# Kernel tuning notes

Measured on AMD Instinct MI355X. Metric: run time of the kernel, lower is better.

Reference implementation:

```python
import jax, jax.numpy as jnp
import numpy as np

N = 100000      # nodes
E = 1600000     # edges (avg degree 16)
D = 128         # in_feats
C = 40          # n_classes
K = 4           # propagation steps
T = 2.0
DELTA = T / K   # 0.5
EPS = 1e-5      # LayerNorm eps


def setup_inputs() -> dict:
    key = jax.random.key(0)
    k1, k2, k3, k4, k5 = jax.random.split(key, 5)
    feat = jax.random.normal(k1, (N, D), jnp.float32)
    row = jax.random.randint(k2, (E,), 0, N, dtype=jnp.int32)
    col = jax.random.randint(k3, (E,), 0, N, dtype=jnp.int32)
    # fc: Linear(D -> C), xavier-ish scale
    W = jax.random.normal(k4, (C, D), jnp.float32) / np.sqrt(D)
    b = jax.random.normal(k5, (C,), jnp.float32) * 0.01
    # LayerNorm params
    gamma = jnp.ones((C,), jnp.float32)
    beta = jnp.zeros((C,), jnp.float32)
    return {"feat": feat, "row": row, "col": col, "W": W, "b": b,
            "gamma": gamma, "beta": beta}


def reference(feat, row, col, W, b, gamma, beta):
    # degrees of augmented adjacency A + I (row counts + self loop)
    deg = jnp.zeros((N,), feat.dtype).at[row].add(1.0) + 1.0
    dinv = jax.lax.rsqrt(deg)
    w_edge = dinv[row] * dinv[col]     # S[row,col] for off-diagonal entries
    w_self = dinv * dinv               # S[i,i] from the added self loop
    # h <- ((1-delta) I + delta S)^K @ feat, applied iteratively (same math as
    # precomputing the matrix power, but never materializes it)
    h = feat
    for _ in range(K):
        agg = jax.ops.segment_sum(h[col] * w_edge[:, None], row, num_segments=N)
        agg = agg + h * w_self[:, None]
        h = (1.0 - DELTA) * h + DELTA * agg
    # fc
    h = h @ W.T + b                    # [N, C]
    # LayerNorm over last dim
    mu = jnp.mean(h, axis=-1, keepdims=True)
    var = jnp.var(h, axis=-1, keepdims=True)
    h = (h - mu) * jax.lax.rsqrt(var + EPS) * gamma + beta
    return h
```

## Files before the change

kernel.cpp:

```cpp
#include <hip/hip_runtime.h>
#include <hip/hip_fp16.h>

#define N_NODES 100000
#define N_EDGES 1600000
#define D_FEAT  128
#define C_CLS   40
#define ZSTRIDE 32
#define LN_EPS  1e-5f

#define RPB   256
#define NBKT  ((N_NODES + RPB - 1) / RPB)
#define BCAP  6144
#define TILE_E 4096
#define EBLK  ((N_EDGES + TILE_E - 1) / TILE_E)
#define NTILES (N_NODES / 16)
#define FCB   ((NTILES + 3) / 4)

typedef __attribute__((ext_vector_type(8))) _Float16 half8;
typedef __attribute__((ext_vector_type(4))) float floatx4;
typedef __attribute__((ext_vector_type(2))) float floatx2;
typedef __attribute__((ext_vector_type(2))) int   intx2;
typedef __attribute__((ext_vector_type(4))) unsigned uintx4;

__device__ inline float2 h2f2(unsigned v) {
    __half2 h = *(__half2*)&v;
    return __half22float2(h);
}
__device__ inline unsigned f2h2(float x, float y) {
    __half2 h = __floats2half2_rn(x, y);
    return *(unsigned*)&h;
}

__global__ __launch_bounds__(256) void init_k(const float* __restrict__ W,
                                              _Float16* __restrict__ wh,
                                              int* __restrict__ bktsz,
                                              unsigned* __restrict__ z0,
                                              unsigned* __restrict__ z1) {
    int t = threadIdx.x;
    if (blockIdx.x < 20) {
        int i = blockIdx.x * 256 + t;
        if (i < C_CLS * D_FEAT) wh[i] = (_Float16)W[i];
        return;
    }
    for (int i = t; i < NBKT; i += 256) bktsz[i] = 0;
    if (t < ZSTRIDE) {
        z0[(size_t)N_NODES * ZSTRIDE + t] = 0u;
        z1[(size_t)N_NODES * ZSTRIDE + t] = 0u;
    }
}

__global__ __launch_bounds__(256) void fcbin_k(const float* __restrict__ feat,
                                               const _Float16* __restrict__ wh,
                                               const int* __restrict__ row,
                                               const int* __restrict__ col,
                                               int* __restrict__ bktsz,
                                               int* __restrict__ csr_tmp,
                                               unsigned* __restrict__ z) {
    __shared__ int hist[NBKT];
    __shared__ int cbase[NBKT];
    __shared__ _Float16 zl[4][16][72];
    int t = threadIdx.x;
    if (blockIdx.x < EBLK) {
        int tile = blockIdx.x * TILE_E;
        for (int i = t; i < NBKT; i += 256) hist[i] = 0;
        __syncthreads();
        int r[16], c[16], pos[16];
        #pragma unroll
        for (int k = 0; k < 16; k++) {
            int e = tile + k * 256 + t;
            if (e < N_EDGES) {
                r[k] = row[e]; c[k] = col[e];
                pos[k] = atomicAdd(&hist[r[k] / RPB], 1);
            } else r[k] = -1;
        }
        __syncthreads();
        for (int i = t; i < NBKT; i += 256) {
            int h = hist[i];
            cbase[i] = h ? atomicAdd(&bktsz[i], h) : 0;
        }
        __syncthreads();
        #pragma unroll
        for (int k = 0; k < 16; k++) {
            if (r[k] >= 0) {
                int b = r[k] / RPB;
                int slot = cbase[b] + pos[k];
                if (slot < BCAP)
                    csr_tmp[b * BCAP + slot] = ((r[k] & (RPB - 1)) << 17) | c[k];
            }
        }
        return;
    }
    int wave = t >> 6, lane = t & 63;
    int m = lane & 15, quad = lane >> 4;
    int tile = (blockIdx.x - EBLK) * 4 + wave;
    bool valid = (tile < NTILES);
    int node0 = tile * 16;

    half8 bfrag[3][4];
    if (valid) {
        const half8* wh8 = (const half8*)wh;
        #pragma unroll
        for (int ct = 0; ct < 3; ct++) {
            int c = ct * 16 + m;
            bool ok = (c < C_CLS);
            #pragma unroll
            for (int ks = 0; ks < 4; ks++) {
                if (ok) {
                    bfrag[ct][ks] = wh8[c * 16 + ks * 4 + quad];
                } else {
                    #pragma unroll
                    for (int j = 0; j < 8; j++) bfrag[ct][ks][j] = (_Float16)0.0f;
                }
            }
        }
    }

    floatx4 acc0 = {0.f,0.f,0.f,0.f}, acc1 = acc0, acc2 = acc0;
    if (valid) {
        #pragma unroll
        for (int ks = 0; ks < 4; ks++) {
            const float4* ap = (const float4*)&feat[(node0 + m) * D_FEAT + ks * 32 + quad * 8];
            float4 a0 = ap[0], a1 = ap[1];
            half8 afrag;
            afrag[0] = (_Float16)a0.x; afrag[1] = (_Float16)a0.y;
            afrag[2] = (_Float16)a0.z; afrag[3] = (_Float16)a0.w;
            afrag[4] = (_Float16)a1.x; afrag[5] = (_Float16)a1.y;
            afrag[6] = (_Float16)a1.z; afrag[7] = (_Float16)a1.w;
            acc0 = __builtin_amdgcn_mfma_f32_16x16x32_f16(afrag, bfrag[0][ks], acc0, 0, 0, 0);
            acc1 = __builtin_amdgcn_mfma_f32_16x16x32_f16(afrag, bfrag[1][ks], acc1, 0, 0, 0);
            acc2 = __builtin_amdgcn_mfma_f32_16x16x32_f16(afrag, bfrag[2][ks], acc2, 0, 0, 0);
        }
    }

    {
        int zr = lane >> 2;
        uint2 zz = make_uint2(0u, 0u);
        ((uint2*)&zl[wave][zr][48])[lane & 3] = zz;
    }
    if (valid) {
        #pragma unroll
        for (int r = 0; r < 4; r++) {
            int zrow = quad * 4 + r;
            zl[wave][zrow][m]      = (_Float16)acc0[r];
            zl[wave][zrow][16 + m] = (_Float16)acc1[r];
            zl[wave][zrow][32 + m] = (_Float16)acc2[r];
        }
    }
    __syncthreads();
    if (valid) {
        int zr = lane >> 2, part = lane & 3;
        uint4 v0 = ((uint4*)&zl[wave][zr][0])[part];
        uint4 v1 = ((uint4*)&zl[wave][zr][0])[part + 4];
        uint4* zg = (uint4*)z;
        zg[(size_t)(node0 + zr) * 8 + part]     = v0;
        zg[(size_t)(node0 + zr) * 8 + part + 4] = v1;
    }
}

__global__ __launch_bounds__(256) void refine_k(const int* __restrict__ csr_tmp,
                                                const int* __restrict__ bktsz,
                                                int2* __restrict__ rowinfo,
                                                float2* __restrict__ rowc,
                                                int* __restrict__ csr_col,
                                                unsigned* __restrict__ z) {
    __shared__ int hist[RPB];
    __shared__ int psc[RPB];
    __shared__ int cur[RPB];
    __shared__ float dl[RPB];
    int b = blockIdx.x, t = threadIdx.x;
    int r0 = b * RPB;
    int nrows = min(RPB, N_NODES - r0);
    hist[t] = 0;
    __syncthreads();
    int cnt = bktsz[b];
    const int* base = csr_tmp + b * BCAP;
    for (int i = t; i < cnt; i += 256)
        atomicAdd(&hist[base[i] >> 17], 1);
    __syncthreads();
    int v = hist[t];
    psc[t] = v;
    __syncthreads();
    for (int off = 1; off < 256; off <<= 1) {
        int x = (t >= off) ? psc[t - off] : 0;
        __syncthreads();
        psc[t] += x;
        __syncthreads();
    }
    int start = b * BCAP + psc[t] - v;
    cur[t] = start;
    float fdeg = (float)v + 1.0f;
    float inv  = 1.0f / fdeg;
    dl[t] = rsqrtf(fdeg);
    if (t < nrows) {
        rowinfo[r0 + t] = make_int2(start, start + v);
        rowc[r0 + t]    = make_float2(0.5f + 0.5f * inv,
                                      0.5f * inv);
    }
    __syncthreads();
    for (int i = t; i < cnt; i += 256) {
        int pk = base[i];
        int lr = pk >> 17;
        int p = atomicAdd(&cur[lr], 1);
        csr_col[p] = pk & 0x1FFFF;
    }
    int total = nrows * ZSTRIDE;
    unsigned* zb = z + (size_t)r0 * ZSTRIDE;
    for (int i = t; i < total; i += 256) {
        float s = dl[i >> 5];
        float2 f = h2f2(zb[i]);
        zb[i] = f2h2(f.x * s, f.y * s);
    }
}

template<bool FINAL>
__global__ __launch_bounds__(256) void prop_u_t(const unsigned* __restrict__ hin,
                                                unsigned* __restrict__ hout,
                                                const int2* __restrict__ rowinfo,
                                                const float2* __restrict__ rowc,
                                                const int* __restrict__ csr_col,
                                                const float* __restrict__ bias,
                                                const float* __restrict__ gamma,
                                                const float* __restrict__ beta,
                                                float* __restrict__ out) {
    int t = threadIdx.x;
    int wave = t >> 6, lane = t & 63;
    int q   = lane >> 3;
    int sub = lane & 7;
    int node = blockIdx.x * 32 + wave * 8 + q;
    const uintx4* hin4 = (const uintx4*)hin;

    uintx4 hv = hin4[(unsigned)node * 8 + sub];
    floatx2 rc = __builtin_nontemporal_load((const floatx2*)rowc + node);
    float acc[8] = {0.f,0.f,0.f,0.f,0.f,0.f,0.f,0.f};

    intx2 ri = __builtin_nontemporal_load((const intx2*)rowinfo + node);
    int j = ri.x, end = ri.y;
    int base = ri.x;

    int e[8];
    #pragma unroll
    for (int k = 0; k < 8; k++)
        e[k] = __builtin_nontemporal_load(csr_col + ((j + k < end) ? j + k : base));

    while (__any(j < end)) {
        uintx4 g[8];
        #pragma unroll
        for (int k = 0; k < 8; k++) {
            int c = (j + k < end) ? e[k] : N_NODES;
            g[k] = hin4[(unsigned)c * 8 + sub];
        }
        int j2 = j + 8;
        #pragma unroll
        for (int k = 0; k < 8; k++)
            e[k] = __builtin_nontemporal_load(csr_col + ((j2 + k < end) ? j2 + k : base));
        #pragma unroll
        for (int k = 0; k < 8; k++) {
            float2 f0 = h2f2(g[k].x), f1 = h2f2(g[k].y), f2 = h2f2(g[k].z), f3 = h2f2(g[k].w);
            acc[0] += f0.x; acc[1] += f0.y;
            acc[2] += f1.x; acc[3] += f1.y;
            acc[4] += f2.x; acc[5] += f2.y;
            acc[6] += f3.x; acc[7] += f3.y;
        }
        j = j2;
    }

    float2 h0 = h2f2(hv.x), h1 = h2f2(hv.y), h2 = h2f2(hv.z), h3 = h2f2(hv.w);
    float r8[8];
    r8[0] = rc.x * h0.x + rc.y * acc[0]; r8[1] = rc.x * h0.y + rc.y * acc[1];
    r8[2] = rc.x * h1.x + rc.y * acc[2]; r8[3] = rc.x * h1.y + rc.y * acc[3];
    r8[4] = rc.x * h2.x + rc.y * acc[4]; r8[5] = rc.x * h2.y + rc.y * acc[5];
    r8[6] = rc.x * h3.x + rc.y * acc[6]; r8[7] = rc.x * h3.y + rc.y * acc[7];

    if (!FINAL) {
        uintx4 o;
        o.x = f2h2(r8[0], r8[1]);
        o.y = f2h2(r8[2], r8[3]);
        o.z = f2h2(r8[4], r8[5]);
        o.w = f2h2(r8[6], r8[7]);
        ((uintx4*)hout)[(unsigned)node * 8 + sub] = o;
    } else {
        float fs = rsqrtf(2.0f * rc.x - 1.0f);
        bool realsub = (sub < 5);
        int cb = sub * 8;
        float vv[8];
        float s = 0.0f, ss = 0.0f;
        #pragma unroll
        for (int i = 0; i < 8; i++) {
            float x = realsub ? (fs * r8[i] + bias[cb + i]) : 0.0f;
            vv[i] = x;
            s += x; ss += x * x;
        }
        s  += __shfl_xor(s, 1);  s  += __shfl_xor(s, 2);  s  += __shfl_xor(s, 4);
        ss += __shfl_xor(ss, 1); ss += __shfl_xor(ss, 2); ss += __shfl_xor(ss, 4);
        float mean = s * (1.0f / C_CLS);
        float var  = ss * (1.0f / C_CLS) - mean * mean;
        float inv  = rsqrtf(var + LN_EPS);
        if (realsub) {
            float o8[8];
            #pragma unroll
            for (int i = 0; i < 8; i++)
                o8[i] = (vv[i] - mean) * inv * gamma[cb + i] + beta[cb + i];
            float* orow = out + (size_t)node * C_CLS + cb;
            ((float4*)orow)[0] = make_float4(o8[0], o8[1], o8[2], o8[3]);
            ((float4*)orow)[1] = make_float4(o8[4], o8[5], o8[6], o8[7]);
        }
    }
}

extern "C" void kernel_launch(void* const* d_in, const int* in_sizes, int n_in,
                              void* d_out, int out_size, void* d_ws, size_t ws_size,
                              hipStream_t stream) {
    const float* feat  = (const float*)d_in[0];
    const int*   row   = (const int*)d_in[1];
    const int*   col   = (const int*)d_in[2];
    const float* W     = (const float*)d_in[3];
    const float* b     = (const float*)d_in[4];
    const float* gamma = (const float*)d_in[5];
    const float* beta  = (const float*)d_in[6];
    float* out = (float*)d_out;

    char* ws = (char*)d_ws;
    size_t off = 0;
    auto alloc = [&](size_t bytes) {
        size_t o = off;
        off = (off + bytes + 255) & ~(size_t)255;
        return o;
    };
    float2*   rowc     = (float2*)  (ws + alloc((size_t)N_NODES * 8));
    int2*     rowinfo  = (int2*)    (ws + alloc((size_t)N_NODES * 8));
    int*      bktsz    = (int*)     (ws + alloc((size_t)NBKT * 4));
    _Float16* wh       = (_Float16*)(ws + alloc((size_t)C_CLS * D_FEAT * 2));
    int*      csr_tmp  = (int*)     (ws + alloc((size_t)NBKT * BCAP * 4));
    int*      csr_col  = (int*)     (ws + alloc((size_t)NBKT * BCAP * 4));
    unsigned* z0       = (unsigned*)(ws + alloc((size_t)(N_NODES + 8) * ZSTRIDE * 4));
    unsigned* z1       = (unsigned*)(ws + alloc((size_t)(N_NODES + 8) * ZSTRIDE * 4));

    init_k<<<21, 256, 0, stream>>>(W, wh, bktsz, z0, z1);
    fcbin_k<<<EBLK + FCB, 256, 0, stream>>>(feat, wh, row, col, bktsz, csr_tmp, z0);
    refine_k<<<NBKT, 256, 0, stream>>>(csr_tmp, bktsz, rowinfo, rowc, csr_col, z0);

    int pgrid = N_NODES / 32;
    prop_u_t<false><<<pgrid, 256, 0, stream>>>(z0, z1, rowinfo, rowc, csr_col,
                                               nullptr, nullptr, nullptr, nullptr);
    prop_u_t<false><<<pgrid, 256, 0, stream>>>(z1, z0, rowinfo, rowc, csr_col,
                                               nullptr, nullptr, nullptr, nullptr);
    prop_u_t<false><<<pgrid, 256, 0, stream>>>(z0, z1, rowinfo, rowc, csr_col,
                                               nullptr, nullptr, nullptr, nullptr);
    prop_u_t<true><<<pgrid, 256, 0, stream>>>(z1, nullptr, rowinfo, rowc, csr_col,
                                              b, gamma, beta, out);
}
```

Baseline: 293.3 us.

## Split padded fp16 node features into compact lo/hi planes to cut gather bytes

The fp16 node-feature buffer changes from 128 bytes per node (40 used features padded to 64) to two planes: 32 features in a 64-byte row, and the remaining 8 features in a separate 16-byte-per-node region. The FC writer, the degree-scaling pass, the init code and the propagation gathers are all updated to address the two planes. This shrinks both the random-gather traffic and the working set of each propagation step. The nontemporal loads on the CSR and row metadata become ordinary loads. Lanes for sub-blocks 5–7 now redundantly load the hi plane, and the hi plane needs an extra 16-byte access per neighbour.

```diff
diff --git a/kernel.cpp b/kernel.cpp
--- a/kernel.cpp
+++ b/kernel.cpp
@@ -5,7 +5,6 @@
 #define N_EDGES 1600000
 #define D_FEAT  128
 #define C_CLS   40
-#define ZSTRIDE 32
 #define LN_EPS  1e-5f
 
 #define RPB   256
@@ -16,10 +15,12 @@
 #define NTILES (N_NODES / 16)
 #define FCB   ((NTILES + 3) / 4)
 
+#define ZPAD  8
+#define QLO   ((N_NODES + ZPAD) * 4)
+#define ZBYTES ((size_t)(N_NODES + ZPAD) * 80)
+
 typedef __attribute__((ext_vector_type(8))) _Float16 half8;
 typedef __attribute__((ext_vector_type(4))) float floatx4;
-typedef __attribute__((ext_vector_type(2))) float floatx2;
-typedef __attribute__((ext_vector_type(2))) int   intx2;
 typedef __attribute__((ext_vector_type(4))) unsigned uintx4;
 
 __device__ inline float2 h2f2(unsigned v) {
@@ -43,9 +44,13 @@
         return;
     }
     for (int i = t; i < NBKT; i += 256) bktsz[i] = 0;
-    if (t < ZSTRIDE) {
-        z0[(size_t)N_NODES * ZSTRIDE + t] = 0u;
-        z1[(size_t)N_NODES * ZSTRIDE + t] = 0u;
+    if (t < 16) {
+        z0[(size_t)N_NODES * 16 + t] = 0u;
+        z1[(size_t)N_NODES * 16 + t] = 0u;
+    }
+    if (t < 4) {
+        z0[(size_t)QLO * 4 + (size_t)N_NODES * 4 + t] = 0u;
+        z1[(size_t)QLO * 4 + (size_t)N_NODES * 4 + t] = 0u;
     }
 }
 
@@ -132,11 +137,6 @@
         }
     }
 
-    {
-        int zr = lane >> 2;
-        uint2 zz = make_uint2(0u, 0u);
-        ((uint2*)&zl[wave][zr][48])[lane & 3] = zz;
-    }
     if (valid) {
         #pragma unroll
         for (int r = 0; r < 4; r++) {
@@ -149,11 +149,12 @@
     __syncthreads();
     if (valid) {
         int zr = lane >> 2, part = lane & 3;
-        uint4 v0 = ((uint4*)&zl[wave][zr][0])[part];
-        uint4 v1 = ((uint4*)&zl[wave][zr][0])[part + 4];
-        uint4* zg = (uint4*)z;
-        zg[(size_t)(node0 + zr) * 8 + part]     = v0;
-        zg[(size_t)(node0 + zr) * 8 + part + 4] = v1;
+        uint4 lo = ((uint4*)&zl[wave][zr][0])[part];
+        ((uint4*)z)[(size_t)(node0 + zr) * 4 + part] = lo;
+        if (part == 0) {
+            uint4 hi = *(uint4*)&zl[wave][zr][32];
+            ((uint4*)z)[QLO + node0 + zr] = hi;
+        }
     }
 }
 
@@ -203,12 +204,19 @@
         int p = atomicAdd(&cur[lr], 1);
         csr_col[p] = pk & 0x1FFFF;
     }
-    int total = nrows * ZSTRIDE;
-    unsigned* zb = z + (size_t)r0 * ZSTRIDE;
-    for (int i = t; i < total; i += 256) {
-        float s = dl[i >> 5];
-        float2 f = h2f2(zb[i]);
-        zb[i] = f2h2(f.x * s, f.y * s);
+    int totlo = nrows * 16;
+    unsigned* zlo = z + (size_t)r0 * 16;
+    for (int i = t; i < totlo; i += 256) {
+        float s = dl[i >> 4];
+        float2 f = h2f2(zlo[i]);
+        zlo[i] = f2h2(f.x * s, f.y * s);
+    }
+    int tothi = nrows * 4;
+    unsigned* zhi = z + (size_t)QLO * 4 + (size_t)r0 * 4;
+    for (int i = t; i < tothi; i += 256) {
+        float s = dl[i >> 2];
+        float2 f = h2f2(zhi[i]);
+        zhi[i] = f2h2(f.x * s, f.y * s);
     }
 }
 
@@ -229,30 +237,33 @@
     int node = blockIdx.x * 32 + wave * 8 + q;
     const uintx4* hin4 = (const uintx4*)hin;
 
-    uintx4 hv = hin4[(unsigned)node * 8 + sub];
-    floatx2 rc = __builtin_nontemporal_load((const floatx2*)rowc + node);
+    int mul  = (sub < 4) ? 4 : 1;
+    int badd = (sub < 4) ? sub : QLO;
+
+    uintx4 hv = hin4[(size_t)node * mul + badd];
+    float2 rc = rowc[node];
     float acc[8] = {0.f,0.f,0.f,0.f,0.f,0.f,0.f,0.f};
 
-    intx2 ri = __builtin_nontemporal_load((const intx2*)rowinfo + node);
+    int2 ri = rowinfo[node];
     int j = ri.x, end = ri.y;
     int base = ri.x;
 
     int e[8];
     #pragma unroll
     for (int k = 0; k < 8; k++)
-        e[k] = __builtin_nontemporal_load(csr_col + ((j + k < end) ? j + k : base));
+        e[k] = csr_col[(j + k < end) ? j + k : base];
 
     while (__any(j < end)) {
         uintx4 g[8];
         #pragma unroll
         for (int k = 0; k < 8; k++) {
             int c = (j + k < end) ? e[k] : N_NODES;
-            g[k] = hin4[(unsigned)c * 8 + sub];
+            g[k] = hin4[(size_t)c * mul + badd];
         }
         int j2 = j + 8;
         #pragma unroll
         for (int k = 0; k < 8; k++)
-            e[k] = __builtin_nontemporal_load(csr_col + ((j2 + k < end) ? j2 + k : base));
+            e[k] = csr_col[(j2 + k < end) ? j2 + k : base];
         #pragma unroll
         for (int k = 0; k < 8; k++) {
             float2 f0 = h2f2(g[k].x), f1 = h2f2(g[k].y), f2 = h2f2(g[k].z), f3 = h2f2(g[k].w);
@@ -272,12 +283,14 @@
     r8[6] = rc.x * h3.x + rc.y * acc[6]; r8[7] = rc.x * h3.y + rc.y * acc[7];
 
     if (!FINAL) {
-        uintx4 o;
-        o.x = f2h2(r8[0], r8[1]);
-        o.y = f2h2(r8[2], r8[3]);
-        o.z = f2h2(r8[4], r8[5]);
-        o.w = f2h2(r8[6], r8[7]);
-        ((uintx4*)hout)[(unsigned)node * 8 + sub] = o;
+        if (sub < 5) {
+            uintx4 o;
+            o.x = f2h2(r8[0], r8[1]);
+            o.y = f2h2(r8[2], r8[3]);
+            o.z = f2h2(r8[4], r8[5]);
+            o.w = f2h2(r8[6], r8[7]);
+            ((uintx4*)hout)[(size_t)node * mul + badd] = o;
+        }
     } else {
         float fs = rsqrtf(2.0f * rc.x - 1.0f);
         bool realsub = (sub < 5);
@@ -332,8 +345,8 @@
     _Float16* wh       = (_Float16*)(ws + alloc((size_t)C_CLS * D_FEAT * 2));
     int*      csr_tmp  = (int*)     (ws + alloc((size_t)NBKT * BCAP * 4));
     int*      csr_col  = (int*)     (ws + alloc((size_t)NBKT * BCAP * 4));
-    unsigned* z0       = (unsigned*)(ws + alloc((size_t)(N_NODES + 8) * ZSTRIDE * 4));
-    unsigned* z1       = (unsigned*)(ws + alloc((size_t)(N_NODES + 8) * ZSTRIDE * 4));
+    unsigned* z0       = (unsigned*)(ws + alloc(ZBYTES));
+    unsigned* z1       = (unsigned*)(ws + alloc(ZBYTES));
 
     init_k<<<21, 256, 0, stream>>>(W, wh, bktsz, z0, z1);
     fcbin_k<<<EBLK + FCB, 256, 0, stream>>>(feat, wh, row, col, bktsz, csr_tmp, z0);
```

Measured after the change: 268.9 us. 8.3% less time.
